# Kernel optimization log

Hardware: AMD Instinct MI355X
Metric: run time of the kernel (lower is better)

## Reference

```python
import jax, jax.numpy as jnp
import numpy as np

DT_MIN, DT_MAX, DT_SCALE = 0.001, 0.1, 1.0
B_SZ, S, D, N, R = 4, 2048, 2048, 16, 512


def setup_inputs() -> dict:
    key = jax.random.key(0)
    ks = jax.random.split(key, 6)
    x = jax.random.normal(ks[0], (B_SZ, S, D), dtype=jnp.float32)
    # A_log is randn in the original; shift by -5 so A=exp(A_log) is small and
    # the recurrence h = exp(delta*A)*h + xB stays finite over 2048 steps.
    A_log = jax.random.normal(ks[1], (N,), dtype=jnp.float32) - 5.0
    B = 0.1 * jax.random.normal(ks[2], (D, N), dtype=jnp.float32)
    C = 0.1 * jax.random.normal(ks[3], (N, D), dtype=jnp.float32)
    dt_w = jax.random.uniform(ks[4], (R, D), dtype=jnp.float32, minval=-0.5, maxval=0.5)
    dt_b = jnp.zeros((R,), dtype=jnp.float32)
    dt_pw = jax.random.uniform(ks[5], (R, N), dtype=jnp.float32, minval=-0.5, maxval=0.5)
    return {"x": x, "A_log": A_log, "B": B, "C": C, "dt_w": dt_w, "dt_b": dt_b, "dt_pw": dt_pw}


def reference(x, A_log, B, C, dt_w, dt_b, dt_pw):
    # delta projection: Linear(d_model -> dt_rank) then (dt_rank -> d_state)
    delta = jnp.einsum('bsd,rd->bsr', x, dt_w) + dt_b          # (b, s, r)
    delta = jnp.einsum('bsr,rn->bsn', delta, dt_pw)            # (b, s, n)
    delta = DT_MIN + (DT_MAX - DT_MIN) * jax.nn.sigmoid(delta * DT_SCALE)
    A = jnp.exp(A_log)                                          # (n,)
    A_bar = jnp.exp(delta * A)                                  # (b, s, n)
    xB = jnp.einsum('bsd,dn->bsn', x, B)                        # (b, s, n)

    def step(h, inp):
        a_t, xb_t = inp                                         # each (b, n)
        h = a_t * h + xb_t
        return h, h

    h0 = jnp.zeros((x.shape[0], A.shape[0]), dtype=x.dtype)
    _, hs = jax.lax.scan(step, h0, (jnp.swapaxes(A_bar, 0, 1), jnp.swapaxes(xB, 0, 1)))
    # hs: (s, b, n); project states through C -> (b, s, d_model)
    y = jnp.einsum('sbn,nm->bsm', hs, C)
    return y  # dropout p=0.0 -> identity
```

## Files before the change

### kernel.cpp

```cpp
#include <hip/hip_runtime.h>
#include <hip/hip_bf16.h>

typedef unsigned short u16;
typedef unsigned int u32;
typedef short s8v __attribute__((ext_vector_type(8)));
typedef float f4v __attribute__((ext_vector_type(4)));

#define DMODEL 2048

__device__ __forceinline__ u16 f2bf(float f) {
  unsigned u = __float_as_uint(f);
  u += 0x7fffu + ((u >> 16) & 1u);
  return (u16)(u >> 16);
}

__device__ __forceinline__ u32 pkbf(float lo, float hi) {
  __hip_bfloat162 h = __float22bfloat162_rn(make_float2(lo, hi));
  return *reinterpret_cast<const u32*>(&h);
}

__global__ __launch_bounds__(256) void build_wc(const float* __restrict__ dtw,
                                                const float* __restrict__ dtpw,
                                                const float* __restrict__ dtb,
                                                const float* __restrict__ Bm,
                                                u16* __restrict__ Wcb,
                                                float* __restrict__ bias2) {
  __shared__ float spw[512 * 16];
  __shared__ float sdw[64][16];
  const int t = threadIdx.x;
  const int k0 = blockIdx.x * 16;
  for (int i = t; i < 2048; i += 256)
    *(float4*)&spw[i * 4] = *(const float4*)&dtpw[i * 4];
  const int kk = t >> 4, n = t & 15;
  const int srr = t >> 2, sc4 = (t & 3) * 4;
  float acc = 0.f;
  for (int rc = 0; rc < 8; ++rc) {
    __syncthreads();
    *(float4*)&sdw[srr][sc4] = *(const float4*)&dtw[(rc * 64 + srr) * DMODEL + k0 + sc4];
    __syncthreads();
#pragma unroll 8
    for (int rr = 0; rr < 64; ++rr)
      acc += sdw[rr][kk] * spw[(rc * 64 + rr) * 16 + n];
  }
  Wcb[n * DMODEL + k0 + kk] = f2bf(acc);
  Wcb[(16 + n) * DMODEL + k0 + kk] = f2bf(Bm[(k0 + kk) * 16 + n]);
  if (blockIdx.x == 0 && t < 16) {
    float s0 = 0.f, s1 = 0.f;
    for (int r = 0; r < 512; r += 2) {
      s0 += dtb[r] * spw[r * 16 + t];
      s1 += dtb[r + 1] * spw[(r + 1) * 16 + t];
    }
    bias2[t] = s0 + s1;
  }
}

__global__ __launch_bounds__(512) void fused_main(const float* __restrict__ x,
                                                  const u16* __restrict__ Wcb,
                                                  const float* __restrict__ bias2,
                                                  const float* __restrict__ Alog,
                                                  float* __restrict__ abar_t,
                                                  float* __restrict__ xb_t,
                                                  float* __restrict__ As,
                                                  float* __restrict__ Xs) {
  __shared__ float red[8][8][64];
  __shared__ float aL[16][17], xL[16][17];
  const int t = threadIdx.x, w = t >> 6, l = t & 63;
  const int lr = l & 15, lh = l >> 4;
  const int row0 = blockIdx.x * 16;
  const int k0 = w * 256;

  f4v acc0 = {0.f, 0.f, 0.f, 0.f}, acc1 = {0.f, 0.f, 0.f, 0.f};
  const float* xp  = x + (long)(row0 + lr) * DMODEL + k0 + lh * 8;
  const u16*   wp0 = Wcb + lr * DMODEL + k0 + lh * 8;
  const u16*   wp1 = Wcb + (16 + lr) * DMODEL + k0 + lh * 8;

#pragma unroll
  for (int ks = 0; ks < 8; ++ks) {
    f4v u0 = __builtin_nontemporal_load((const f4v*)(xp + ks * 32));
    f4v u1 = __builtin_nontemporal_load((const f4v*)(xp + ks * 32 + 4));
    union { u32 d[4]; s8v v; } pa;
    pa.d[0] = pkbf(u0[0], u0[1]); pa.d[1] = pkbf(u0[2], u0[3]);
    pa.d[2] = pkbf(u1[0], u1[1]); pa.d[3] = pkbf(u1[2], u1[3]);
    s8v b0 = *(const s8v*)(wp0 + ks * 32);
    s8v b1 = *(const s8v*)(wp1 + ks * 32);
    acc0 = __builtin_amdgcn_mfma_f32_16x16x32_bf16(pa.v, b0, acc0, 0, 0, 0);
    acc1 = __builtin_amdgcn_mfma_f32_16x16x32_bf16(pa.v, b1, acc1, 0, 0, 0);
  }
#pragma unroll
  for (int q = 0; q < 4; ++q) { red[q][w][l] = acc0[q]; red[4 + q][w][l] = acc1[q]; }
  __syncthreads();

  float s = 0.f;
#pragma unroll
  for (int ww = 0; ww < 8; ++ww) s += red[w][ww][l];

  const int n = lr;
  const int row = lh * 4 + (w & 3);
  const int b = row0 >> 11, srow = row0 & 2047;
  const long idx = ((long)b * 16 + n) * 2048 + srow + row;
  if (w < 4) {
    float d2 = s + bias2[n];
    float sig = 1.f / (1.f + __expf(-d2));
    float delta = 0.001f + 0.099f * sig;
    float av = __expf(delta * __expf(Alog[n]));
    abar_t[idx] = av;
    aL[row][n] = av;
  } else {
    xb_t[idx] = s;
    xL[row][n] = s;
  }
  __syncthreads();
  if (t < 16) {
    float A = 1.f, X = 0.f;
#pragma unroll
    for (int r = 0; r < 16; ++r) {
      float a = aL[r][t];
      X = a * X + xL[r][t];
      A *= a;
    }
    const int chunk = srow >> 4;
    As[((long)b * 16 + t) * 128 + chunk] = A;
    Xs[((long)b * 16 + t) * 128 + chunk] = X;
  }
}

__global__ __launch_bounds__(256) void scan_sum(const float* __restrict__ As,
                                                const float* __restrict__ Xs,
                                                float* __restrict__ H0) {
  const int t = threadIdx.x, w = t >> 6, lane = t & 63;
  const long bn = blockIdx.x * 4 + w;
  float a0 = As[bn * 128 + 2 * lane], x0 = Xs[bn * 128 + 2 * lane];
  float a1 = As[bn * 128 + 2 * lane + 1], x1 = Xs[bn * 128 + 2 * lane + 1];
  float Ac = a1 * a0, Xc = a1 * x0 + x1;
#pragma unroll
  for (int d = 1; d < 64; d <<= 1) {
    float pa = __shfl_up(Ac, d);
    float px = __shfl_up(Xc, d);
    if (lane >= d) { Xc = Ac * px + Xc; Ac = Ac * pa; }
  }
  float Xprev = __shfl_up(Xc, 1);
  if (lane == 0) Xprev = 0.f;
  H0[bn * 128 + 2 * lane]     = Xprev;
  H0[bn * 128 + 2 * lane + 1] = a0 * Xprev + x0;
}

__global__ __launch_bounds__(512) void proj(const float* __restrict__ abar_t,
                                            const float* __restrict__ xb_t,
                                            const float* __restrict__ H0,
                                            const float* __restrict__ C,
                                            float* __restrict__ y) {
  __shared__ float sh[32 * 16];
  __shared__ float sa[16][32], sx[16][32];
  const int t = threadIdx.x;
  const int bB = blockIdx.x >> 6;
  const int s0 = (blockIdx.x & 63) * 32;
  const long row0 = (long)blockIdx.x * 32;
  {
    const int n = t >> 5, ss = t & 31;
    const long bn = (long)bB * 16 + n;
    sa[n][ss] = abar_t[bn * 2048 + s0 + ss];
    sx[n][ss] = xb_t[bn * 2048 + s0 + ss];
  }
  float4 c[16];
#pragma unroll
  for (int nn = 0; nn < 16; ++nn) c[nn] = *(const float4*)&C[nn * DMODEL + t * 4];
  __syncthreads();
  if (t < 32) {
    const int n = t & 15, cc = t >> 4;
    const long bn = (long)bB * 16 + n;
    float h = H0[bn * 128 + (s0 >> 4) + cc];
#pragma unroll
    for (int i = 0; i < 16; ++i) {
      int r = cc * 16 + i;
      h = sa[n][r] * h + sx[n][r];
      sh[r * 16 + n] = h;
    }
  }
  __syncthreads();
#pragma unroll 4
  for (int r = 0; r < 32; ++r) {
    const float* h = &sh[r * 16];
    f4v o = {0.f, 0.f, 0.f, 0.f};
#pragma unroll
    for (int nn = 0; nn < 16; ++nn) {
      float hv = h[nn];
      o[0] += hv * c[nn].x; o[1] += hv * c[nn].y;
      o[2] += hv * c[nn].z; o[3] += hv * c[nn].w;
    }
    __builtin_nontemporal_store(o, (f4v*)&y[(row0 + r) * DMODEL + t * 4]);
  }
}

extern "C" void kernel_launch(void* const* d_in, const int* in_sizes, int n_in,
                              void* d_out, int out_size, void* d_ws, size_t ws_size,
                              hipStream_t stream) {
  const float* x    = (const float*)d_in[0];
  const float* Alog = (const float*)d_in[1];
  const float* Bm   = (const float*)d_in[2];
  const float* Cm   = (const float*)d_in[3];
  const float* dtw  = (const float*)d_in[4];
  const float* dtb  = (const float*)d_in[5];
  const float* dtpw = (const float*)d_in[6];
  float* y = (float*)d_out;

  char* w = (char*)d_ws;
  u16*   Wcb   = (u16*)w;   w += (size_t)32 * DMODEL * 2;
  float* bias2 = (float*)w; w += 256;
  float* ab_t  = (float*)w; w += (size_t)64 * 2048 * 4;
  float* xb_t  = (float*)w; w += (size_t)64 * 2048 * 4;
  float* As    = (float*)w; w += (size_t)64 * 128 * 4;
  float* Xs    = (float*)w; w += (size_t)64 * 128 * 4;
  float* H0    = (float*)w; w += (size_t)64 * 128 * 4;

  build_wc<<<128, 256, 0, stream>>>(dtw, dtpw, dtb, Bm, Wcb, bias2);
  fused_main<<<512, 512, 0, stream>>>(x, Wcb, bias2, Alog, ab_t, xb_t, As, Xs);
  scan_sum<<<16, 256, 0, stream>>>(As, Xs, H0);
  proj<<<256, 512, 0, stream>>>(ab_t, xb_t, H0, Cm, y);
}
```

Baseline: 53.73 us.

## Fuse chunk scan and output projection into one kernel with decoupled look-back

```diff
diff --git a/kernel.cpp b/kernel.cpp
--- a/kernel.cpp
+++ b/kernel.cpp
@@ -3,6 +3,7 @@
 
 typedef unsigned short u16;
 typedef unsigned int u32;
+typedef unsigned long long u64;
 typedef short s8v __attribute__((ext_vector_type(8)));
 typedef float f4v __attribute__((ext_vector_type(4)));
 
@@ -24,11 +25,13 @@
                                                 const float* __restrict__ dtb,
                                                 const float* __restrict__ Bm,
                                                 u16* __restrict__ Wcb,
-                                                float* __restrict__ bias2) {
+                                                float* __restrict__ bias2,
+                                                u32* __restrict__ status) {
   __shared__ float spw[512 * 16];
   __shared__ float sdw[64][16];
   const int t = threadIdx.x;
   const int k0 = blockIdx.x * 16;
+  if (blockIdx.x < 2) status[blockIdx.x * 256 + t] = 0u;
   for (int i = t; i < 2048; i += 256)
     *(float4*)&spw[i * 4] = *(const float4*)&dtpw[i * 4];
   const int kk = t >> 4, n = t & 15;
@@ -54,26 +57,29 @@
   }
 }
 
-__global__ __launch_bounds__(512) void fused_main(const float* __restrict__ x,
-                                                  const u16* __restrict__ Wcb,
-                                                  const float* __restrict__ bias2,
-                                                  const float* __restrict__ Alog,
-                                                  float* __restrict__ abar_t,
-                                                  float* __restrict__ xb_t,
-                                                  float* __restrict__ As,
-                                                  float* __restrict__ Xs) {
+__global__ __launch_bounds__(512) void mega(const float* __restrict__ x,
+                                            const u16* __restrict__ Wcb,
+                                            const float* __restrict__ bias2,
+                                            const float* __restrict__ Alog,
+                                            const float* __restrict__ C,
+                                            u64* __restrict__ agg,
+                                            u32* __restrict__ status,
+                                            float* __restrict__ y) {
   __shared__ float red[8][8][64];
   __shared__ float aL[16][17], xL[16][17];
+  __shared__ float sAX[128][16][2];
+  __shared__ float sh[16][16];
   const int t = threadIdx.x, w = t >> 6, l = t & 63;
   const int lr = l & 15, lh = l >> 4;
-  const int row0 = blockIdx.x * 16;
+  const int bid = blockIdx.x;
+  const int b = bid >> 7, c = bid & 127;
+  const long row0 = (long)bid * 16;
+
+  f4v acc0 = {0.f, 0.f, 0.f, 0.f}, acc1 = {0.f, 0.f, 0.f, 0.f};
   const int k0 = w * 256;
-
-  f4v acc0 = {0.f, 0.f, 0.f, 0.f}, acc1 = {0.f, 0.f, 0.f, 0.f};
-  const float* xp  = x + (long)(row0 + lr) * DMODEL + k0 + lh * 8;
+  const float* xp  = x + (row0 + lr) * DMODEL + k0 + lh * 8;
   const u16*   wp0 = Wcb + lr * DMODEL + k0 + lh * 8;
   const u16*   wp1 = Wcb + (16 + lr) * DMODEL + k0 + lh * 8;
-
 #pragma unroll
   for (int ks = 0; ks < 8; ++ks) {
     f4v u0 = __builtin_nontemporal_load((const f4v*)(xp + ks * 32));
@@ -89,27 +95,23 @@
 #pragma unroll
   for (int q = 0; q < 4; ++q) { red[q][w][l] = acc0[q]; red[4 + q][w][l] = acc1[q]; }
   __syncthreads();
-
-  float s = 0.f;
-#pragma unroll
-  for (int ww = 0; ww < 8; ++ww) s += red[w][ww][l];
-
-  const int n = lr;
-  const int row = lh * 4 + (w & 3);
-  const int b = row0 >> 11, srow = row0 & 2047;
-  const long idx = ((long)b * 16 + n) * 2048 + srow + row;
-  if (w < 4) {
-    float d2 = s + bias2[n];
-    float sig = 1.f / (1.f + __expf(-d2));
-    float delta = 0.001f + 0.099f * sig;
-    float av = __expf(delta * __expf(Alog[n]));
-    abar_t[idx] = av;
-    aL[row][n] = av;
-  } else {
-    xb_t[idx] = s;
-    xL[row][n] = s;
-  }
-  __syncthreads();
+  {
+    float s = 0.f;
+#pragma unroll
+    for (int ww = 0; ww < 8; ++ww) s += red[w][ww][l];
+    const int n = lr;
+    const int row = lh * 4 + (w & 3);
+    if (w < 4) {
+      float d2 = s + bias2[n];
+      float sig = 1.f / (1.f + __expf(-d2));
+      float delta = 0.001f + 0.099f * sig;
+      aL[row][n] = __expf(delta * __expf(Alog[n]));
+    } else {
+      xL[row][n] = s;
+    }
+  }
+  __syncthreads();
+
   if (t < 16) {
     float A = 1.f, X = 0.f;
 #pragma unroll
@@ -118,75 +120,63 @@
       X = a * X + xL[r][t];
       A *= a;
     }
-    const int chunk = srow >> 4;
-    As[((long)b * 16 + t) * 128 + chunk] = A;
-    Xs[((long)b * 16 + t) * 128 + chunk] = X;
-  }
-}
-
-__global__ __launch_bounds__(256) void scan_sum(const float* __restrict__ As,
-                                                const float* __restrict__ Xs,
-                                                float* __restrict__ H0) {
-  const int t = threadIdx.x, w = t >> 6, lane = t & 63;
-  const long bn = blockIdx.x * 4 + w;
-  float a0 = As[bn * 128 + 2 * lane], x0 = Xs[bn * 128 + 2 * lane];
-  float a1 = As[bn * 128 + 2 * lane + 1], x1 = Xs[bn * 128 + 2 * lane + 1];
-  float Ac = a1 * a0, Xc = a1 * x0 + x1;
-#pragma unroll
-  for (int d = 1; d < 64; d <<= 1) {
-    float pa = __shfl_up(Ac, d);
-    float px = __shfl_up(Xc, d);
-    if (lane >= d) { Xc = Ac * px + Xc; Ac = Ac * pa; }
-  }
-  float Xprev = __shfl_up(Xc, 1);
-  if (lane == 0) Xprev = 0.f;
-  H0[bn * 128 + 2 * lane]     = Xprev;
-  H0[bn * 128 + 2 * lane + 1] = a0 * Xprev + x0;
-}
-
-__global__ __launch_bounds__(512) void proj(const float* __restrict__ abar_t,
-                                            const float* __restrict__ xb_t,
-                                            const float* __restrict__ H0,
-                                            const float* __restrict__ C,
-                                            float* __restrict__ y) {
-  __shared__ float sh[32 * 16];
-  __shared__ float sa[16][32], sx[16][32];
-  const int t = threadIdx.x;
-  const int bB = blockIdx.x >> 6;
-  const int s0 = (blockIdx.x & 63) * 32;
-  const long row0 = (long)blockIdx.x * 32;
+    u64 v = (u64)__float_as_uint(A) | ((u64)__float_as_uint(X) << 32);
+    __hip_atomic_store(&agg[(u64)bid * 16 + t], v, __ATOMIC_RELAXED, __HIP_MEMORY_SCOPE_AGENT);
+  }
+  __syncthreads();
+  if (t == 0)
+    __hip_atomic_store(&status[bid], 1u, __ATOMIC_RELEASE, __HIP_MEMORY_SCOPE_AGENT);
+
   {
-    const int n = t >> 5, ss = t & 31;
-    const long bn = (long)bB * 16 + n;
-    sa[n][ss] = abar_t[bn * 2048 + s0 + ss];
-    sx[n][ss] = xb_t[bn * 2048 + s0 + ss];
-  }
-  float4 c[16];
-#pragma unroll
-  for (int nn = 0; nn < 16; ++nn) c[nn] = *(const float4*)&C[nn * DMODEL + t * 4];
-  __syncthreads();
-  if (t < 32) {
-    const int n = t & 15, cc = t >> 4;
-    const long bn = (long)bB * 16 + n;
-    float h = H0[bn * 128 + (s0 >> 4) + cc];
-#pragma unroll
-    for (int i = 0; i < 16; ++i) {
-      int r = cc * 16 + i;
-      h = sa[n][r] * h + sx[n][r];
-      sh[r * 16 + n] = h;
-    }
-  }
-  __syncthreads();
-#pragma unroll 4
-  for (int r = 0; r < 32; ++r) {
-    const float* h = &sh[r * 16];
+    const int j = t >> 2, n0 = (t & 3) * 4;
+    if (j < c) {
+      while (__hip_atomic_load(&status[b * 128 + j], __ATOMIC_ACQUIRE,
+                               __HIP_MEMORY_SCOPE_AGENT) == 0u)
+        __builtin_amdgcn_s_sleep(1);
+#pragma unroll
+      for (int q = 0; q < 4; ++q) {
+        u64 v = __hip_atomic_load(&agg[((u64)b * 128 + j) * 16 + n0 + q],
+                                  __ATOMIC_RELAXED, __HIP_MEMORY_SCOPE_AGENT);
+        sAX[j][n0 + q][0] = __uint_as_float((u32)v);
+        sAX[j][n0 + q][1] = __uint_as_float((u32)(v >> 32));
+      }
+    } else {
+#pragma unroll
+      for (int q = 0; q < 4; ++q) { sAX[j][n0 + q][0] = 1.f; sAX[j][n0 + q][1] = 0.f; }
+    }
+  }
+  __syncthreads();
+  for (int st = 1; st < 128; st <<= 1) {
+    const int cnt = (128 / (2 * st)) * 16;
+    for (int idx = t; idx < cnt; idx += 512) {
+      const int jj = (idx >> 4) * 2 * st, n = idx & 15;
+      float A1 = sAX[jj][n][0], X1 = sAX[jj][n][1];
+      float A2 = sAX[jj + st][n][0], X2 = sAX[jj + st][n][1];
+      sAX[jj][n][0] = A2 * A1;
+      sAX[jj][n][1] = A2 * X1 + X2;
+    }
+    __syncthreads();
+  }
+
+  if (t < 16) {
+    float h = sAX[0][t][1];
+#pragma unroll
+    for (int r = 0; r < 16; ++r) {
+      h = aL[r][t] * h + xL[r][t];
+      sh[r][t] = h;
+    }
+  }
+  __syncthreads();
+
+  f4v c16[16];
+#pragma unroll
+  for (int nn = 0; nn < 16; ++nn)
+    c16[nn] = *(const f4v*)&C[nn * DMODEL + t * 4];
+#pragma unroll 2
+  for (int r = 0; r < 16; ++r) {
     f4v o = {0.f, 0.f, 0.f, 0.f};
 #pragma unroll
-    for (int nn = 0; nn < 16; ++nn) {
-      float hv = h[nn];
-      o[0] += hv * c[nn].x; o[1] += hv * c[nn].y;
-      o[2] += hv * c[nn].z; o[3] += hv * c[nn].w;
-    }
+    for (int nn = 0; nn < 16; ++nn) o += sh[r][nn] * c16[nn];
     __builtin_nontemporal_store(o, (f4v*)&y[(row0 + r) * DMODEL + t * 4]);
   }
 }
@@ -204,16 +194,11 @@
   float* y = (float*)d_out;
 
   char* w = (char*)d_ws;
-  u16*   Wcb   = (u16*)w;   w += (size_t)32 * DMODEL * 2;
+  u16*   Wcb   = (u16*)w; w += (size_t)32 * DMODEL * 2;
   float* bias2 = (float*)w; w += 256;
-  float* ab_t  = (float*)w; w += (size_t)64 * 2048 * 4;
-  float* xb_t  = (float*)w; w += (size_t)64 * 2048 * 4;
-  float* As    = (float*)w; w += (size_t)64 * 128 * 4;
-  float* Xs    = (float*)w; w += (size_t)64 * 128 * 4;
-  float* H0    = (float*)w; w += (size_t)64 * 128 * 4;
-
-  build_wc<<<128, 256, 0, stream>>>(dtw, dtpw, dtb, Bm, Wcb, bias2);
-  fused_main<<<512, 512, 0, stream>>>(x, Wcb, bias2, Alog, ab_t, xb_t, As, Xs);
-  scan_sum<<<16, 256, 0, stream>>>(As, Xs, H0);
-  proj<<<256, 512, 0, stream>>>(ab_t, xb_t, H0, Cm, y);
-}
+  u64*   agg   = (u64*)w; w += (size_t)512 * 16 * 8;
+  u32*   stat  = (u32*)w; w += (size_t)512 * 4;
+
+  build_wc<<<128, 256, 0, stream>>>(dtw, dtpw, dtb, Bm, Wcb, bias2, stat);
+  mega<<<512, 512, 0, stream>>>(x, Wcb, bias2, Alog, Cm, agg, stat, y);
+}
```

Result: slower. 104.3 us (+94.2%).

## Fuse chunk-carry scan into projection kernel with redundant per-block LDS scan

Applied to the files above, without the earlier changes.

```diff
diff --git a/kernel.cpp b/kernel.cpp
--- a/kernel.cpp
+++ b/kernel.cpp
@@ -124,69 +124,75 @@
   }
 }
 
-__global__ __launch_bounds__(256) void scan_sum(const float* __restrict__ As,
-                                                const float* __restrict__ Xs,
-                                                float* __restrict__ H0) {
-  const int t = threadIdx.x, w = t >> 6, lane = t & 63;
-  const long bn = blockIdx.x * 4 + w;
-  float a0 = As[bn * 128 + 2 * lane], x0 = Xs[bn * 128 + 2 * lane];
-  float a1 = As[bn * 128 + 2 * lane + 1], x1 = Xs[bn * 128 + 2 * lane + 1];
-  float Ac = a1 * a0, Xc = a1 * x0 + x1;
-#pragma unroll
-  for (int d = 1; d < 64; d <<= 1) {
-    float pa = __shfl_up(Ac, d);
-    float px = __shfl_up(Xc, d);
-    if (lane >= d) { Xc = Ac * px + Xc; Ac = Ac * pa; }
-  }
-  float Xprev = __shfl_up(Xc, 1);
-  if (lane == 0) Xprev = 0.f;
-  H0[bn * 128 + 2 * lane]     = Xprev;
-  H0[bn * 128 + 2 * lane + 1] = a0 * Xprev + x0;
-}
-
-__global__ __launch_bounds__(512) void proj(const float* __restrict__ abar_t,
-                                            const float* __restrict__ xb_t,
-                                            const float* __restrict__ H0,
-                                            const float* __restrict__ C,
-                                            float* __restrict__ y) {
-  __shared__ float sh[32 * 16];
-  __shared__ float sa[16][32], sx[16][32];
+__global__ __launch_bounds__(512) void scan_proj(const float* __restrict__ abar_t,
+                                                 const float* __restrict__ xb_t,
+                                                 const float* __restrict__ As,
+                                                 const float* __restrict__ Xs,
+                                                 const float* __restrict__ C,
+                                                 float* __restrict__ y) {
+  __shared__ float sc[2][128][16][2];
+  __shared__ float sa[16][16], sx[16][16], sh[16][16];
   const int t = threadIdx.x;
-  const int bB = blockIdx.x >> 6;
-  const int s0 = (blockIdx.x & 63) * 32;
-  const long row0 = (long)blockIdx.x * 32;
+  const int bid = blockIdx.x, b = bid >> 7, c = bid & 127;
+  const long row0 = (long)bid * 16;
+  const int s0 = c * 16;
+
+  f4v c16[16];
+#pragma unroll
+  for (int nn = 0; nn < 16; ++nn)
+    c16[nn] = *(const f4v*)&C[nn * DMODEL + t * 4];
+
+  if (t < 256) {
+    const int n = t >> 4, r = t & 15;
+    const long bn = (long)b * 16 + n;
+    sa[r][n] = abar_t[bn * 2048 + s0 + r];
+    sx[r][n] = xb_t[bn * 2048 + s0 + r];
+  }
   {
-    const int n = t >> 5, ss = t & 31;
-    const long bn = (long)bB * 16 + n;
-    sa[n][ss] = abar_t[bn * 2048 + s0 + ss];
-    sx[n][ss] = xb_t[bn * 2048 + s0 + ss];
-  }
-  float4 c[16];
-#pragma unroll
-  for (int nn = 0; nn < 16; ++nn) c[nn] = *(const float4*)&C[nn * DMODEL + t * 4];
-  __syncthreads();
-  if (t < 32) {
-    const int n = t & 15, cc = t >> 4;
-    const long bn = (long)bB * 16 + n;
-    float h = H0[bn * 128 + (s0 >> 4) + cc];
-#pragma unroll
-    for (int i = 0; i < 16; ++i) {
-      int r = cc * 16 + i;
-      h = sa[n][r] * h + sx[n][r];
-      sh[r * 16 + n] = h;
-    }
-  }
-  __syncthreads();
-#pragma unroll 4
-  for (int r = 0; r < 32; ++r) {
-    const float* h = &sh[r * 16];
+    const int n = t >> 5, j0 = (t & 31) * 4;
+    const long bn = (long)b * 16 + n;
+    float4 va = *(const float4*)&As[bn * 128 + j0];
+    float4 vx = *(const float4*)&Xs[bn * 128 + j0];
+    sc[0][j0 + 0][n][0] = va.x; sc[0][j0 + 0][n][1] = vx.x;
+    sc[0][j0 + 1][n][0] = va.y; sc[0][j0 + 1][n][1] = vx.y;
+    sc[0][j0 + 2][n][0] = va.z; sc[0][j0 + 2][n][1] = vx.z;
+    sc[0][j0 + 3][n][0] = va.w; sc[0][j0 + 3][n][1] = vx.w;
+  }
+  __syncthreads();
+
+  int src = 0;
+  for (int d = 1; d < 128; d <<= 1) {
+#pragma unroll
+    for (int q = 0; q < 4; ++q) {
+      const int idx = t + q * 512;
+      const int j = idx >> 4, n = idx & 15;
+      float A = sc[src][j][n][0], X = sc[src][j][n][1];
+      if (j >= d) {
+        float Ap = sc[src][j - d][n][0], Xp = sc[src][j - d][n][1];
+        X = A * Xp + X;
+        A = A * Ap;
+      }
+      sc[src ^ 1][j][n][0] = A; sc[src ^ 1][j][n][1] = X;
+    }
+    __syncthreads();
+    src ^= 1;
+  }
+
+  if (t < 16) {
+    float h = (c == 0) ? 0.f : sc[src][c - 1][t][1];
+#pragma unroll
+    for (int r = 0; r < 16; ++r) {
+      h = sa[r][t] * h + sx[r][t];
+      sh[r][t] = h;
+    }
+  }
+  __syncthreads();
+
+#pragma unroll 2
+  for (int r = 0; r < 16; ++r) {
     f4v o = {0.f, 0.f, 0.f, 0.f};
 #pragma unroll
-    for (int nn = 0; nn < 16; ++nn) {
-      float hv = h[nn];
-      o[0] += hv * c[nn].x; o[1] += hv * c[nn].y;
-      o[2] += hv * c[nn].z; o[3] += hv * c[nn].w;
-    }
+    for (int nn = 0; nn < 16; ++nn) o += sh[r][nn] * c16[nn];
     __builtin_nontemporal_store(o, (f4v*)&y[(row0 + r) * DMODEL + t * 4]);
   }
 }
@@ -204,16 +210,14 @@
   float* y = (float*)d_out;
 
   char* w = (char*)d_ws;
-  u16*   Wcb   = (u16*)w;   w += (size_t)32 * DMODEL * 2;
+  u16*   Wcb   = (u16*)w; w += (size_t)32 * DMODEL * 2;
   float* bias2 = (float*)w; w += 256;
   float* ab_t  = (float*)w; w += (size_t)64 * 2048 * 4;
   float* xb_t  = (float*)w; w += (size_t)64 * 2048 * 4;
   float* As    = (float*)w; w += (size_t)64 * 128 * 4;
   float* Xs    = (float*)w; w += (size_t)64 * 128 * 4;
-  float* H0    = (float*)w; w += (size_t)64 * 128 * 4;
 
   build_wc<<<128, 256, 0, stream>>>(dtw, dtpw, dtb, Bm, Wcb, bias2);
   fused_main<<<512, 512, 0, stream>>>(x, Wcb, bias2, Alog, ab_t, xb_t, As, Xs);
-  scan_sum<<<16, 256, 0, stream>>>(As, Xs, H0);
-  proj<<<256, 512, 0, stream>>>(ab_t, xb_t, H0, Cm, y);
-}
+  scan_proj<<<512, 512, 0, stream>>>(ab_t, xb_t, As, Xs, Cm, y);
+}
```

Measured after the change: 55.30 us. 2.9% more time.
